# Performance work log

Hardware: AMD Instinct MI355X
Metric: run time of the kernel (lower is better)

The kernel has to match this reference:

```python
import jax, jax.numpy as jnp
import numpy as np

N_NODES = 100000
N_EDGES = 1600000
IN_DIM = 128
HID = 128
OUT_DIM = 64
EPS = 1e-8


def setup_inputs() -> dict:
    key = jax.random.key(0)
    ks = jax.random.split(key, 10)
    x = jax.random.normal(ks[0], (N_NODES, IN_DIM), dtype=jnp.float32)
    edge_index = jax.random.randint(ks[1], (2, N_EDGES), 0, N_NODES, dtype=jnp.int64)
    edge_attr = jax.random.uniform(ks[2], (N_EDGES, 4), dtype=jnp.float32)
    s1 = 1.0 / np.sqrt(IN_DIM)
    s2 = 1.0 / np.sqrt(HID)
    sr = 1.0 / np.sqrt(2 * HID)
    W1 = jax.random.normal(ks[3], (HID, IN_DIM), dtype=jnp.float32) * s1
    b1 = jnp.zeros((HID,), dtype=jnp.float32)
    W2 = jax.random.normal(ks[4], (HID, HID), dtype=jnp.float32) * s2
    b2 = jnp.zeros((HID,), dtype=jnp.float32)
    Wr = jax.random.normal(ks[5], (OUT_DIM, 2 * HID), dtype=jnp.float32) * sr
    br = jnp.zeros((OUT_DIM,), dtype=jnp.float32)
    return {"x": x, "edge_index": edge_index, "edge_attr": edge_attr,
            "W1": W1, "b1": b1, "W2": W2, "b2": b2, "Wr": Wr, "br": br}


def _edge_weight_from_attr_auto(edge_attr):
    # mean over features, min-max normalize, invert, clamp >= 0
    m = edge_attr.mean(axis=-1)                      # [E]
    m_min, m_max = m.min(), m.max()
    m_norm = (m - m_min) / (m_max - m_min + EPS)
    w = jnp.where(m_max - m_min > EPS, 1.0 - m_norm, jnp.ones_like(m))
    return jnp.clip(w, 0.0)


def reference(x, edge_index, edge_attr, W1, b1, W2, b2, Wr, br):
    N = x.shape[0]
    row, col = edge_index[0], edge_index[1]          # source -> target
    ew = _edge_weight_from_attr_auto(edge_attr)      # [E]
    # GCN normalization with self-loops (self-loop weight = 1.0)
    deg = jax.ops.segment_sum(ew, col, num_segments=N) + 1.0   # [N]
    dis = jax.lax.rsqrt(deg)                         # deg >= 1
    norm = dis[row] * ew * dis[col]                  # [E]

    def gcn(h, W, b):
        hW = h @ W.T                                 # [N, d_out]
        agg = jax.ops.segment_sum(norm[:, None] * hW[row], col, num_segments=N)
        # self-loop contribution: dis[i] * 1.0 * dis[i] * hW[i]
        return agg + (dis * dis)[:, None] * hW + b

    # dropout in eval mode -> identity
    h1 = jax.nn.relu(gcn(x, W1, b1))                 # [N, HID]
    h2 = jax.nn.relu(gcn(h1, W2, b2))                # [N, HID]
    hcat = jnp.concatenate([h1, h2], axis=-1)        # [N, 2*HID] (JK concat)
    return hcat @ Wr.T + br                          # residue-level [N, OUT_DIM]
```

## Files before the change

kernel.cpp:

```cpp
#include <hip/hip_runtime.h>

#define NN 100000
#define NE 1600000
#define HID 128
#define ODIM 64
#define NBK 196
#define BSHIFT 9
#define BINB 200
#define CVTB 8
#define GEMMB 782
#define CHUNK 8000
#define BITER 8
#define BINCAP 12288
#define SMAX 8588
#define LMAX 2148

typedef unsigned int u32;
typedef unsigned short u16;
typedef __bf16 bf16x8 __attribute__((ext_vector_type(8)));
typedef float f32x4 __attribute__((ext_vector_type(4)));
typedef float f32x2 __attribute__((ext_vector_type(2)));

__device__ __forceinline__ float bf_lo(u32 p){ return __uint_as_float(p << 16); }
__device__ __forceinline__ float bf_hi(u32 p){ return __uint_as_float(p & 0xffff0000u); }
__device__ __forceinline__ u16 f2bf(float f){
  u32 u = __float_as_uint(f);
  u += 0x7fffu + ((u >> 16) & 1u);
  return (u16)(u >> 16);
}
__device__ __forceinline__ bf16x8 ld8bf(const u16* p){ return *(const bf16x8*)p; }
__device__ __forceinline__ bf16x8 cvt8(const float* p){
  union { bf16x8 v; u16 s[8]; } r;
#pragma unroll
  for (int i = 0; i < 8; i++) r.s[i] = f2bf(p[i]);
  return r.v;
}

__device__ __forceinline__ void wparams(const u32* minmax, float* A, float* B){
  u32 mnq = 32767u - minmax[0];
  u32 mxq = minmax[1];
  u32 rngq = mxq - mnq;
  float inv = rngq ? 1.f / ((float)rngq * (1.f / 32767.f) + 1e-8f) : 0.f;
  *A = 1.f + (float)mnq * (1.f / 32767.f) * inv;
  *B = inv * (1.f / 32767.f);
}

__global__ __launch_bounds__(1024, 8) void k_front(
    const float* __restrict__ eattr, const int* __restrict__ erow,
    const int* __restrict__ ecol, u32* __restrict__ bcur,
    u32* __restrict__ binA, u16* __restrict__ binM, u32* __restrict__ minmax,
    const float* __restrict__ x, const float* __restrict__ W1,
    const float* __restrict__ W2, const float* __restrict__ Wr,
    u16* __restrict__ W2b, u16* __restrict__ Wrb, u16* __restrict__ graw){
  int tid = threadIdx.x;
  int bid = blockIdx.x;
  if (bid >= BINB + CVTB){
    int gblk = bid - BINB - CVTB;
    int wv = tid >> 6, lane = tid & 63;
    int mg = wv >> 2, ng = wv & 3;
    int m0 = gblk * 128 + mg * 32;
    int m = lane & 15, q = lane >> 4;
    const float* a0f = x + (size_t)min(m0 + m, NN - 1) * HID;
    const float* a1f = x + (size_t)min(m0 + 16 + m, NN - 1) * HID;
    const float* brow0 = W1 + (size_t)(ng * 16 + m) * HID;
    const float* brow1 = brow0 + (size_t)64 * HID;
    f32x4 acc00 = {0.f,0.f,0.f,0.f}, acc01 = {0.f,0.f,0.f,0.f};
    f32x4 acc10 = {0.f,0.f,0.f,0.f}, acc11 = {0.f,0.f,0.f,0.f};
#pragma unroll
    for (int kb = 0; kb < HID; kb += 32){
      bf16x8 af0 = cvt8(a0f + kb + q * 8);
      bf16x8 af1 = cvt8(a1f + kb + q * 8);
      bf16x8 bf0 = cvt8(brow0 + kb + q * 8);
      bf16x8 bf1 = cvt8(brow1 + kb + q * 8);
      acc00 = __builtin_amdgcn_mfma_f32_16x16x32_bf16(af0, bf0, acc00, 0, 0, 0);
      acc01 = __builtin_amdgcn_mfma_f32_16x16x32_bf16(af0, bf1, acc01, 0, 0, 0);
      acc10 = __builtin_amdgcn_mfma_f32_16x16x32_bf16(af1, bf0, acc10, 0, 0, 0);
      acc11 = __builtin_amdgcn_mfma_f32_16x16x32_bf16(af1, bf1, acc11, 0, 0, 0);
    }
#pragma unroll
    for (int r = 0; r < 4; r++){
      int row0 = m0 + q * 4 + r, row1 = m0 + 16 + q * 4 + r;
      if (row0 < NN){
        u16* c0 = graw + (size_t)row0 * HID + ng * 16 + m;
        c0[0]  = f2bf(acc00[r]);
        c0[64] = f2bf(acc01[r]);
      }
      if (row1 < NN){
        u16* c1 = graw + (size_t)row1 * HID + ng * 16 + m;
        c1[0]  = f2bf(acc10[r]);
        c1[64] = f2bf(acc11[r]);
      }
    }
    return;
  }
  if (bid >= BINB){
    int i = (bid - BINB) * 1024 + tid;
    const float* src; u16* dst; int off;
    if (i < 4096){ src = W2; dst = W2b; off = i; }
    else { src = Wr; dst = Wrb; off = i - 4096; }
    float4 v = ((const float4*)src)[off];
    uint2 o;
    o.x = (u32)f2bf(v.x) | ((u32)f2bf(v.y) << 16);
    o.y = (u32)f2bf(v.z) | ((u32)f2bf(v.w) << 16);
    ((uint2*)dst)[off] = o;
    return;
  }
  __shared__ u32 lcnt[8 * NBK], wof[8 * NBK];
  __shared__ u32 lofs[NBK], gb[NBK];
  __shared__ u32 wtot[4];
  __shared__ u16 lmap[LMAX];
  __shared__ u32 stageA[SMAX];
  __shared__ u16 stageM[SMAX];
  __shared__ u32 Tt;
  __shared__ u32 sMn[16], sMx[16];
  for (int t = tid; t < 8 * NBK; t += 1024) lcnt[t] = 0;
  __syncthreads();
  int base = bid * CHUNK;
  int wv = tid >> 6, lane = tid & 63;
  int grp = tid >> 7;
  u32 pk[BITER];
#pragma unroll
  for (int it = 0; it < BITER; it++){
    int idx = it * 1024 + tid;
    u32 p = 0xFFFFFFFFu;
    if (idx < CHUNK){
      int c = ecol[base + idx];
      if ((u32)c < NN){
        u32 b = (u32)c >> BSHIFT;
        u32 r = atomicAdd(&lcnt[grp * NBK + b], 1u);
        p = (b << 22) | (((u32)c & 511u) << 13) | r;
      }
    }
    pk[it] = p;
  }
  __syncthreads();
  u32 na = 0;
  if (tid < NBK){
    u32 run = 0;
#pragma unroll
    for (int g = 0; g < 8; g++){
      wof[g * NBK + tid] = run;
      run += lcnt[g * NBK + tid];
    }
    na = (run + 3u) & ~3u;
    lofs[tid] = run;
  }
  u32 incl = na;
  if (tid < 256){
    for (int off = 1; off < 64; off <<= 1){
      u32 t = (u32)__shfl_up((int)incl, off);
      if (lane >= off) incl += t;
    }
    if (lane == 63) wtot[wv] = incl;
  }
  __syncthreads();
  if (tid < 256){
    u32 pre = 0;
#pragma unroll
    for (int k = 0; k < 4; k++) pre += (k < wv) ? wtot[k] : 0u;
    u32 ex = pre + incl - na;
    if (tid == 255) Tt = pre + incl;
    if (tid < NBK){
      u32 n = lofs[tid];
      lofs[tid] = ex;
      u32 g = 0x80000000u;
      if (na){
        u32 gl = atomicAdd(&bcur[tid], na);
        if (gl + na <= BINCAP) g = (u32)tid * BINCAP + gl;
      }
      gb[tid] = g;
      for (u32 l = ex >> 2; l < (ex + na) >> 2; l++) lmap[l] = (u16)tid;
      for (u32 k = n; k < na; k++){ stageA[ex + k] = 0xFFFFFFFFu; stageM[ex + k] = 0; }
    }
  }
  __syncthreads();
  u32 lmn = 0, lmx = 0;
#pragma unroll
  for (int it = 0; it < BITER; it++){
    int idx = it * 1024 + tid;
    if (idx >= CHUNK) continue;
    int e = base + idx;
    float4 a = ((const float4*)eattr)[e];
    float m = 0.25f * (a.x + a.y + a.z + a.w);
    u32 mq = (u32)(m * 32767.f + 0.5f);
    lmn = max(lmn, 32767u - mq); lmx = max(lmx, mq);
    u32 p = pk[it];
    if (p == 0xFFFFFFFFu) continue;
    u32 s = (u32)erow[e]; if (s >= NN) s = 0;
    u32 b = p >> 22, d = (p >> 13) & 511u, r = p & 8191u;
    u32 slot = lofs[b] + wof[grp * NBK + b] + r;
    stageA[slot] = s | (d << 17);
    stageM[slot] = (u16)mq;
  }
  __syncthreads();
  u32 T = Tt;
  for (u32 i = tid; i < T; i += 1024){
    u32 b = lmap[i >> 2];
    u32 g = gb[b];
    if (g != 0x80000000u){
      u32 o = g + (i - lofs[b]);
      binA[o] = stageA[i];
      binM[o] = stageM[i];
    }
  }
  for (int off = 32; off; off >>= 1){
    lmn = max(lmn, (u32)__shfl_xor((int)lmn, off));
    lmx = max(lmx, (u32)__shfl_xor((int)lmx, off));
  }
  if (lane == 0){ sMn[wv] = lmn; sMx[wv] = lmx; }
  __syncthreads();
  if (tid == 0){
    u32 mn = 0, mx = 0;
#pragma unroll
    for (int k = 0; k < 16; k++){ mn = max(mn, sMn[k]); mx = max(mx, sMx[k]); }
    atomicMax(&minmax[0], mn);
    atomicMax(&minmax[1], mx);
  }
}

__global__ __launch_bounds__(1024) void k_scatter(
    const u32* __restrict__ bcur, const u32* __restrict__ binA,
    const u16* __restrict__ binM, const u32* __restrict__ minmax,
    u32* __restrict__ csr, u32* __restrict__ meta, float* __restrict__ dis){
  __shared__ u32 cntL[512], sumL[512], curL[512];
  __shared__ u32 wtot[8];
  int b = blockIdx.x, tid = threadIdx.x;
  int bb = b * BINCAP;
  int nrec = (int)min(bcur[b], (u32)BINCAP);
  if (tid < 512){ cntL[tid] = 0; sumL[tid] = 0; }
  __syncthreads();
  for (int i = tid; i < nrec; i += 1024){
    u32 a = binA[bb + i];
    if (a == 0xFFFFFFFFu) continue;
    u32 d = (a >> 17) & 511u;
    u32 mq = binM[bb + i];
    atomicAdd(&cntL[d], 1u);
    atomicAdd(&sumL[d], mq);
  }
  __syncthreads();
  float A, B; wparams(minmax, &A, &B);
  int wid = tid >> 6, lane = tid & 63;
  u32 v = 0, incl = 0;
  if (tid < 512){ v = cntL[tid]; incl = v; }
  for (int off = 1; off < 64; off <<= 1){
    u32 t = (u32)__shfl_up((int)incl, off);
    if (lane >= off) incl += t;
  }
  if (tid < 512 && lane == 63) wtot[wid] = incl;
  __syncthreads();
  if (tid < 512){
    u32 pre = 0;
#pragma unroll
    for (int k = 0; k < 8; k++) pre += (k < wid) ? wtot[k] : 0u;
    u32 ex = pre + incl - v;
    curL[tid] = (u32)bb + ex;
    int node = (b << BSHIFT) + tid;
    if (node < NN){
      meta[node] = ((u32)bb + ex) | (v << 22);
      float sw = A * (float)v - B * (float)sumL[tid];
      dis[node] = rsqrtf(1.f + sw);
    }
  }
  __syncthreads();
  for (int i = tid; i < nrec; i += 1024){
    u32 a = binA[bb + i];
    if (a == 0xFFFFFFFFu) continue;
    u32 d = (a >> 17) & 511u;
    u32 mq = binM[bb + i];
    u32 pos = atomicAdd(&curL[d], 1u);
    csr[pos] = (a & 0x1FFFFu) | (mq << 17);
  }
}

__global__ __launch_bounds__(256) void k_gemm128(
    const u16* __restrict__ Ab, const u16* __restrict__ Bt,
    const float* __restrict__ dis, u16* __restrict__ G){
  int wave = threadIdx.x >> 6, lane = threadIdx.x & 63;
  int m0 = blockIdx.x * 32;
  int m = lane & 15, q = lane >> 4;
  const u16* a0b = Ab + (size_t)(m0 + m) * HID;
  const u16* a1b = a0b + (size_t)16 * HID;
  const u16* brow0 = Bt + (size_t)(wave * 16 + m) * HID;
  const u16* brow1 = brow0 + (size_t)64 * HID;
  f32x4 acc00 = {0.f,0.f,0.f,0.f}, acc01 = {0.f,0.f,0.f,0.f};
  f32x4 acc10 = {0.f,0.f,0.f,0.f}, acc11 = {0.f,0.f,0.f,0.f};
#pragma unroll
  for (int kb = 0; kb < HID; kb += 32){
    bf16x8 af0 = ld8bf(a0b + kb + q * 8);
    bf16x8 af1 = ld8bf(a1b + kb + q * 8);
    bf16x8 bf0 = ld8bf(brow0 + kb + q * 8);
    bf16x8 bf1 = ld8bf(brow1 + kb + q * 8);
    acc00 = __builtin_amdgcn_mfma_f32_16x16x32_bf16(af0, bf0, acc00, 0, 0, 0);
    acc01 = __builtin_amdgcn_mfma_f32_16x16x32_bf16(af0, bf1, acc01, 0, 0, 0);
    acc10 = __builtin_amdgcn_mfma_f32_16x16x32_bf16(af1, bf0, acc10, 0, 0, 0);
    acc11 = __builtin_amdgcn_mfma_f32_16x16x32_bf16(af1, bf1, acc11, 0, 0, 0);
  }
  u16* crow0 = G + (size_t)(m0 + q * 4) * HID + wave * 16 + m;
  u16* crow1 = crow0 + (size_t)16 * HID;
#pragma unroll
  for (int r = 0; r < 4; r++){
    float d0 = dis[m0 + q * 4 + r];
    float d1 = dis[m0 + 16 + q * 4 + r];
    crow0[(size_t)r * HID]      = f2bf(acc00[r] * d0);
    crow0[(size_t)r * HID + 64] = f2bf(acc01[r] * d0);
    crow1[(size_t)r * HID]      = f2bf(acc10[r] * d1);
    crow1[(size_t)r * HID + 64] = f2bf(acc11[r] * d1);
  }
}

template <bool FD>
__global__ __launch_bounds__(256) void k_aggregate(
    const u32* __restrict__ meta, const u32* __restrict__ csr,
    const float* __restrict__ dis, const u32* __restrict__ minmax,
    const u16* __restrict__ g, const float* __restrict__ bias,
    u16* __restrict__ hout){
  int node = __builtin_amdgcn_readfirstlane(
      (int)(blockIdx.x * 4 + (threadIdx.x >> 6)));
  int lane = threadIdx.x & 63;
  const u32* gp = (const u32*)g;
  u32 sv = gp[((size_t)node << 6) + lane];
  u32 mw = meta[node];
  float di = dis[node];
  float A, B; wparams(minmax, &A, &B);
  u32 s = mw & 0x3FFFFFu;
  int c = (int)(mw >> 22);
  const u32* cp = csr + s;
  f32x2 acc = {0.f, 0.f};
  int j = 0;
  for (; j + 16 <= c; j += 16){
    u32 p[16];
#pragma unroll
    for (int t = 0; t < 16; t++)
      p[t] = __builtin_amdgcn_readfirstlane(cp[j + t]);
    u32 pv[16];
#pragma unroll
    for (int t = 0; t < 16; t++)
      pv[t] = gp[(size_t)(p[t] & 0x1FFFFu) * 64u + lane];
#pragma unroll
    for (int t = 0; t < 16; t++){
      float wf = A - B * (float)(p[t] >> 17);
      if (FD) wf *= dis[p[t] & 0x1FFFFu];
      f32x2 val = {bf_lo(pv[t]), bf_hi(pv[t])};
      f32x2 w2 = {wf, wf};
      acc += w2 * val;
    }
  }
  for (; j < c; j += 8){
    u32 p[8];
#pragma unroll
    for (int t = 0; t < 8; t++)
      p[t] = __builtin_amdgcn_readfirstlane(cp[j + t]);
    u32 st[8]; float wv[8];
#pragma unroll
    for (int t = 0; t < 8; t++){
      bool ok = (j + t) < c;
      st[t] = ok ? (p[t] & 0x1FFFFu) : 0u;
      float wf = A - B * (float)(p[t] >> 17);
      if (FD) wf *= dis[st[t]];
      wv[t] = ok ? wf : 0.f;
    }
    u32 pv[8];
#pragma unroll
    for (int t = 0; t < 8; t++)
      pv[t] = gp[(size_t)st[t] * 64u + lane];
#pragma unroll
    for (int t = 0; t < 8; t++){
      f32x2 val = {bf_lo(pv[t]), bf_hi(pv[t])};
      f32x2 w2 = {wv[t], wv[t]};
      acc += w2 * val;
    }
  }
  float2 bv = ((const float2*)bias)[lane];
  f32x2 selfv = {bf_lo(sv), bf_hi(sv)};
  float sc = FD ? di : 1.f;
  float o0 = fmaxf((acc.x + sc * selfv.x) * di + bv.x, 0.f);
  float o1 = fmaxf((acc.y + sc * selfv.y) * di + bv.y, 0.f);
  ((u32*)hout)[((size_t)node << 6) + lane] = (u32)f2bf(o0) | ((u32)f2bf(o1) << 16);
}

__global__ __launch_bounds__(256) void k_readout(
    const u16* __restrict__ h1, const u16* __restrict__ h2,
    const u16* __restrict__ Wrb, const float* __restrict__ br, float* __restrict__ out){
  int wave = threadIdx.x >> 6, lane = threadIdx.x & 63;
  int m0 = blockIdx.x * 32;
  int n0 = wave * 16;
  int m = lane & 15, q = lane >> 4;
  const u16* a10 = h1 + (size_t)(m0 + m) * HID;
  const u16* a11 = a10 + (size_t)16 * HID;
  const u16* a20 = h2 + (size_t)(m0 + m) * HID;
  const u16* a21 = a20 + (size_t)16 * HID;
  const u16* b  = Wrb + (size_t)(n0 + m) * (2 * HID);
  f32x4 acc0 = {0.f,0.f,0.f,0.f}, acc1 = {0.f,0.f,0.f,0.f};
#pragma unroll
  for (int kb = 0; kb < HID; kb += 32){
    bf16x8 bf = ld8bf(b + kb + q * 8);
    acc0 = __builtin_amdgcn_mfma_f32_16x16x32_bf16(ld8bf(a10 + kb + q * 8), bf, acc0, 0, 0, 0);
    acc1 = __builtin_amdgcn_mfma_f32_16x16x32_bf16(ld8bf(a11 + kb + q * 8), bf, acc1, 0, 0, 0);
  }
#pragma unroll
  for (int kb = 0; kb < HID; kb += 32){
    bf16x8 bf = ld8bf(b + HID + kb + q * 8);
    acc0 = __builtin_amdgcn_mfma_f32_16x16x32_bf16(ld8bf(a20 + kb + q * 8), bf, acc0, 0, 0, 0);
    acc1 = __builtin_amdgcn_mfma_f32_16x16x32_bf16(ld8bf(a21 + kb + q * 8), bf, acc1, 0, 0, 0);
  }
  float bias = br[n0 + m];
  float* crow0 = out + (size_t)(m0 + q * 4) * ODIM + n0 + m;
  float* crow1 = crow0 + (size_t)16 * ODIM;
#pragma unroll
  for (int r = 0; r < 4; r++){
    crow0[(size_t)r * ODIM] = acc0[r] + bias;
    crow1[(size_t)r * ODIM] = acc1[r] + bias;
  }
}

extern "C" void kernel_launch(void* const* d_in, const int* in_sizes, int n_in,
                              void* d_out, int out_size, void* d_ws, size_t ws_size,
                              hipStream_t stream){
  const float* x     = (const float*)d_in[0];
  const int*   eidx  = (const int*)d_in[1];
  const float* eattr = (const float*)d_in[2];
  const float* W1    = (const float*)d_in[3];
  const float* b1    = (const float*)d_in[4];
  const float* W2    = (const float*)d_in[5];
  const float* b2    = (const float*)d_in[6];
  const float* Wr    = (const float*)d_in[7];
  const float* br    = (const float*)d_in[8];
  const int* erow  = eidx;
  const int* ecol  = eidx + NE;

  char* w = (char*)d_ws;
  auto carve = [&](size_t bytes) -> void* {
    void* p = (void*)w;
    w += (bytes + 255) & ~(size_t)255;
    return p;
  };
  u32* csr       = (u32*)carve((size_t)NBK * BINCAP * 4);
  u32* bcur      = (u32*)carve(1024);
  u32* minmax    = (u32*)carve(256);
  u32* meta      = (u32*)carve((size_t)NN * 4);
  float* dis     = (float*)carve((size_t)NN * 4);
  u16* W2b       = (u16*)carve((size_t)HID * HID * 2);
  u16* Wrb       = (u16*)carve((size_t)ODIM * 2 * HID * 2);
  u16* g         = (u16*)carve((size_t)NN * HID * 2);
  u16* h1        = (u16*)carve((size_t)NN * HID * 2);
  u16* h2        = (u16*)carve((size_t)NN * HID * 2);
  u32* binA      = (u32*)h2;
  u16* binM      = (u16*)((char*)h2 + (size_t)NBK * BINCAP * 4);

  hipMemsetAsync(bcur, 0, 1280, stream);
  k_front<<<BINB + CVTB + GEMMB, 1024, 0, stream>>>(
      eattr, erow, ecol, bcur, binA, binM, minmax,
      x, W1, W2, Wr, W2b, Wrb, g);
  k_scatter<<<NBK, 1024, 0, stream>>>(bcur, binA, binM, minmax, csr, meta, dis);
  k_aggregate<true><<<NN / 4, 256, 0, stream>>>(meta, csr, dis, minmax, g, b1, h1);
  k_gemm128<<<NN / 32, 256, 0, stream>>>(h1, W2b, dis, g);
  k_aggregate<false><<<NN / 4, 256, 0, stream>>>(meta, csr, dis, minmax, g, b2, h2);
  k_readout<<<NN / 32, 256, 0, stream>>>(h1, h2, Wrb, br, (float*)d_out);
}
```

Baseline: 374.3 us.

## Fuse second aggregation with readout GEMM and pack bin records into uint2

Replaces the second aggregate kernel and the readout GEMM with one kernel. Each 1024-thread block aggregates 16 nodes, stages the h1 and h2 rows in shared memory, and runs the MFMA readout there, so h2 is never written to or re-read from global memory. Bin records are now stored as interleaved uint2 (index plus weight) instead of two separate arrays, and scatter histograms are split into four per-group copies to reduce LDS atomic contention. The cost is a larger bin buffer, a block-wide barrier before the readout, and only 4 of 16 waves doing the MFMA work.

Result: faster. 356.3 us (-4.8%).

```diff
diff --git a/kernel.cpp b/kernel.cpp
--- a/kernel.cpp
+++ b/kernel.cpp
@@ -48,7 +48,7 @@
 __global__ __launch_bounds__(1024, 8) void k_front(
     const float* __restrict__ eattr, const int* __restrict__ erow,
     const int* __restrict__ ecol, u32* __restrict__ bcur,
-    u32* __restrict__ binA, u16* __restrict__ binM, u32* __restrict__ minmax,
+    uint2* __restrict__ bin8, u32* __restrict__ minmax,
     const float* __restrict__ x, const float* __restrict__ W1,
     const float* __restrict__ W2, const float* __restrict__ Wr,
     u16* __restrict__ W2b, u16* __restrict__ Wrb, u16* __restrict__ graw){
@@ -198,9 +198,8 @@
     u32 b = lmap[i >> 2];
     u32 g = gb[b];
     if (g != 0x80000000u){
-      u32 o = g + (i - lofs[b]);
-      binA[o] = stageA[i];
-      binM[o] = stageM[i];
+      uint2 rec; rec.x = stageA[i]; rec.y = (u32)stageM[i];
+      bin8[g + (i - lofs[b])] = rec;
     }
   }
   for (int off = 32; off; off >>= 1){
@@ -219,29 +218,34 @@
 }
 
 __global__ __launch_bounds__(1024) void k_scatter(
-    const u32* __restrict__ bcur, const u32* __restrict__ binA,
-    const u16* __restrict__ binM, const u32* __restrict__ minmax,
-    u32* __restrict__ csr, u32* __restrict__ meta, float* __restrict__ dis){
-  __shared__ u32 cntL[512], sumL[512], curL[512];
+    const u32* __restrict__ bcur, const uint2* __restrict__ bin8,
+    const u32* __restrict__ minmax, u32* __restrict__ csr,
+    u32* __restrict__ meta, float* __restrict__ dis){
+  __shared__ u32 cnt4[4 * 512], sum4[4 * 512];
+  __shared__ u32 curL[512];
   __shared__ u32 wtot[8];
   int b = blockIdx.x, tid = threadIdx.x;
+  int grp = tid >> 8;
   int bb = b * BINCAP;
   int nrec = (int)min(bcur[b], (u32)BINCAP);
-  if (tid < 512){ cntL[tid] = 0; sumL[tid] = 0; }
+  for (int t = tid; t < 4 * 512; t += 1024){ cnt4[t] = 0; sum4[t] = 0; }
   __syncthreads();
   for (int i = tid; i < nrec; i += 1024){
-    u32 a = binA[bb + i];
-    if (a == 0xFFFFFFFFu) continue;
-    u32 d = (a >> 17) & 511u;
-    u32 mq = binM[bb + i];
-    atomicAdd(&cntL[d], 1u);
-    atomicAdd(&sumL[d], mq);
+    uint2 r = bin8[bb + i];
+    if (r.x == 0xFFFFFFFFu) continue;
+    u32 d = (r.x >> 17) & 511u;
+    atomicAdd(&cnt4[grp * 512 + d], 1u);
+    atomicAdd(&sum4[grp * 512 + d], r.y);
   }
   __syncthreads();
   float A, B; wparams(minmax, &A, &B);
   int wid = tid >> 6, lane = tid & 63;
-  u32 v = 0, incl = 0;
-  if (tid < 512){ v = cntL[tid]; incl = v; }
+  u32 v = 0, sm = 0, incl = 0;
+  if (tid < 512){
+    v  = cnt4[tid] + cnt4[512 + tid] + cnt4[1024 + tid] + cnt4[1536 + tid];
+    sm = sum4[tid] + sum4[512 + tid] + sum4[1024 + tid] + sum4[1536 + tid];
+    incl = v;
+  }
   for (int off = 1; off < 64; off <<= 1){
     u32 t = (u32)__shfl_up((int)incl, off);
     if (lane >= off) incl += t;
@@ -257,18 +261,17 @@
     int node = (b << BSHIFT) + tid;
     if (node < NN){
       meta[node] = ((u32)bb + ex) | (v << 22);
-      float sw = A * (float)v - B * (float)sumL[tid];
+      float sw = A * (float)v - B * (float)sm;
       dis[node] = rsqrtf(1.f + sw);
     }
   }
   __syncthreads();
   for (int i = tid; i < nrec; i += 1024){
-    u32 a = binA[bb + i];
-    if (a == 0xFFFFFFFFu) continue;
-    u32 d = (a >> 17) & 511u;
-    u32 mq = binM[bb + i];
+    uint2 r = bin8[bb + i];
+    if (r.x == 0xFFFFFFFFu) continue;
+    u32 d = (r.x >> 17) & 511u;
     u32 pos = atomicAdd(&curL[d], 1u);
-    csr[pos] = (a & 0x1FFFFu) | (mq << 17);
+    csr[pos] = (r.x & 0x1FFFFu) | (r.y << 17);
   }
 }
 
@@ -308,7 +311,6 @@
   }
 }
 
-template <bool FD>
 __global__ __launch_bounds__(256) void k_aggregate(
     const u32* __restrict__ meta, const u32* __restrict__ csr,
     const float* __restrict__ dis, const u32* __restrict__ minmax,
@@ -338,8 +340,7 @@
       pv[t] = gp[(size_t)(p[t] & 0x1FFFFu) * 64u + lane];
 #pragma unroll
     for (int t = 0; t < 16; t++){
-      float wf = A - B * (float)(p[t] >> 17);
-      if (FD) wf *= dis[p[t] & 0x1FFFFu];
+      float wf = (A - B * (float)(p[t] >> 17)) * dis[p[t] & 0x1FFFFu];
       f32x2 val = {bf_lo(pv[t]), bf_hi(pv[t])};
       f32x2 w2 = {wf, wf};
       acc += w2 * val;
@@ -355,9 +356,7 @@
     for (int t = 0; t < 8; t++){
       bool ok = (j + t) < c;
       st[t] = ok ? (p[t] & 0x1FFFFu) : 0u;
-      float wf = A - B * (float)(p[t] >> 17);
-      if (FD) wf *= dis[st[t]];
-      wv[t] = ok ? wf : 0.f;
+      wv[t] = ok ? (A - B * (float)(p[t] >> 17)) * dis[st[t]] : 0.f;
     }
     u32 pv[8];
 #pragma unroll
@@ -372,44 +371,93 @@
   }
   float2 bv = ((const float2*)bias)[lane];
   f32x2 selfv = {bf_lo(sv), bf_hi(sv)};
-  float sc = FD ? di : 1.f;
-  float o0 = fmaxf((acc.x + sc * selfv.x) * di + bv.x, 0.f);
-  float o1 = fmaxf((acc.y + sc * selfv.y) * di + bv.y, 0.f);
+  float o0 = fmaxf((acc.x + di * selfv.x) * di + bv.x, 0.f);
+  float o1 = fmaxf((acc.y + di * selfv.y) * di + bv.y, 0.f);
   ((u32*)hout)[((size_t)node << 6) + lane] = (u32)f2bf(o0) | ((u32)f2bf(o1) << 16);
 }
 
-__global__ __launch_bounds__(256) void k_readout(
-    const u16* __restrict__ h1, const u16* __restrict__ h2,
-    const u16* __restrict__ Wrb, const float* __restrict__ br, float* __restrict__ out){
-  int wave = threadIdx.x >> 6, lane = threadIdx.x & 63;
-  int m0 = blockIdx.x * 32;
-  int n0 = wave * 16;
-  int m = lane & 15, q = lane >> 4;
-  const u16* a10 = h1 + (size_t)(m0 + m) * HID;
-  const u16* a11 = a10 + (size_t)16 * HID;
-  const u16* a20 = h2 + (size_t)(m0 + m) * HID;
-  const u16* a21 = a20 + (size_t)16 * HID;
-  const u16* b  = Wrb + (size_t)(n0 + m) * (2 * HID);
-  f32x4 acc0 = {0.f,0.f,0.f,0.f}, acc1 = {0.f,0.f,0.f,0.f};
-#pragma unroll
-  for (int kb = 0; kb < HID; kb += 32){
-    bf16x8 bf = ld8bf(b + kb + q * 8);
-    acc0 = __builtin_amdgcn_mfma_f32_16x16x32_bf16(ld8bf(a10 + kb + q * 8), bf, acc0, 0, 0, 0);
-    acc1 = __builtin_amdgcn_mfma_f32_16x16x32_bf16(ld8bf(a11 + kb + q * 8), bf, acc1, 0, 0, 0);
-  }
-#pragma unroll
-  for (int kb = 0; kb < HID; kb += 32){
-    bf16x8 bf = ld8bf(b + HID + kb + q * 8);
-    acc0 = __builtin_amdgcn_mfma_f32_16x16x32_bf16(ld8bf(a20 + kb + q * 8), bf, acc0, 0, 0, 0);
-    acc1 = __builtin_amdgcn_mfma_f32_16x16x32_bf16(ld8bf(a21 + kb + q * 8), bf, acc1, 0, 0, 0);
-  }
-  float bias = br[n0 + m];
-  float* crow0 = out + (size_t)(m0 + q * 4) * ODIM + n0 + m;
-  float* crow1 = crow0 + (size_t)16 * ODIM;
-#pragma unroll
-  for (int r = 0; r < 4; r++){
-    crow0[(size_t)r * ODIM] = acc0[r] + bias;
-    crow1[(size_t)r * ODIM] = acc1[r] + bias;
+__global__ __launch_bounds__(1024) void k_agg_read(
+    const u32* __restrict__ meta, const u32* __restrict__ csr,
+    const float* __restrict__ dis, const u32* __restrict__ minmax,
+    const u16* __restrict__ g, const float* __restrict__ bias,
+    const u16* __restrict__ h1, const u16* __restrict__ Wrb,
+    const float* __restrict__ br, float* __restrict__ out){
+  __shared__ u16 hc[16][264];
+  int wv = threadIdx.x >> 6, lane = threadIdx.x & 63;
+  int node0 = blockIdx.x * 16;
+  int node = __builtin_amdgcn_readfirstlane(node0 + wv);
+  const u32* gp = (const u32*)g;
+  u32 sv = gp[((size_t)node << 6) + lane];
+  u32 mw = meta[node];
+  float di = dis[node];
+  float A, B; wparams(minmax, &A, &B);
+  u32 s = mw & 0x3FFFFFu;
+  int c = (int)(mw >> 22);
+  const u32* cp = csr + s;
+  f32x2 acc = {0.f, 0.f};
+  int j = 0;
+  for (; j + 16 <= c; j += 16){
+    u32 p[16];
+#pragma unroll
+    for (int t = 0; t < 16; t++)
+      p[t] = __builtin_amdgcn_readfirstlane(cp[j + t]);
+    u32 pv[16];
+#pragma unroll
+    for (int t = 0; t < 16; t++)
+      pv[t] = gp[(size_t)(p[t] & 0x1FFFFu) * 64u + lane];
+#pragma unroll
+    for (int t = 0; t < 16; t++){
+      float wf = A - B * (float)(p[t] >> 17);
+      f32x2 val = {bf_lo(pv[t]), bf_hi(pv[t])};
+      f32x2 w2 = {wf, wf};
+      acc += w2 * val;
+    }
+  }
+  for (; j < c; j += 8){
+    u32 p[8];
+#pragma unroll
+    for (int t = 0; t < 8; t++)
+      p[t] = __builtin_amdgcn_readfirstlane(cp[j + t]);
+    u32 st[8]; float wvv[8];
+#pragma unroll
+    for (int t = 0; t < 8; t++){
+      bool ok = (j + t) < c;
+      st[t] = ok ? (p[t] & 0x1FFFFu) : 0u;
+      wvv[t] = ok ? (A - B * (float)(p[t] >> 17)) : 0.f;
+    }
+    u32 pv[8];
+#pragma unroll
+    for (int t = 0; t < 8; t++)
+      pv[t] = gp[(size_t)st[t] * 64u + lane];
+#pragma unroll
+    for (int t = 0; t < 8; t++){
+      f32x2 val = {bf_lo(pv[t]), bf_hi(pv[t])};
+      f32x2 w2 = {wvv[t], wvv[t]};
+      acc += w2 * val;
+    }
+  }
+  float2 bv = ((const float2*)bias)[lane];
+  f32x2 selfv = {bf_lo(sv), bf_hi(sv)};
+  float o0 = fmaxf((acc.x + selfv.x) * di + bv.x, 0.f);
+  float o1 = fmaxf((acc.y + selfv.y) * di + bv.y, 0.f);
+  u32 h2pk = (u32)f2bf(o0) | ((u32)f2bf(o1) << 16);
+  *(u32*)&hc[wv][2 * lane] = ((const u32*)h1)[((size_t)node << 6) + lane];
+  *(u32*)&hc[wv][128 + 2 * lane] = h2pk;
+  __syncthreads();
+  if (wv < 4){
+    int m = lane & 15, q = lane >> 4;
+    const u16* b = Wrb + (size_t)(wv * 16 + m) * (2 * HID);
+    f32x4 acc4 = {0.f,0.f,0.f,0.f};
+#pragma unroll
+    for (int kb = 0; kb < 2 * HID; kb += 32){
+      bf16x8 af = *(const bf16x8*)&hc[m][kb + q * 8];
+      bf16x8 bf = ld8bf(b + kb + q * 8);
+      acc4 = __builtin_amdgcn_mfma_f32_16x16x32_bf16(af, bf, acc4, 0, 0, 0);
+    }
+    float bb = br[wv * 16 + m];
+#pragma unroll
+    for (int r = 0; r < 4; r++)
+      out[(size_t)(node0 + q * 4 + r) * ODIM + wv * 16 + m] = acc4[r] + bb;
   }
 }
 
@@ -443,17 +491,15 @@
   u16* Wrb       = (u16*)carve((size_t)ODIM * 2 * HID * 2);
   u16* g         = (u16*)carve((size_t)NN * HID * 2);
   u16* h1        = (u16*)carve((size_t)NN * HID * 2);
-  u16* h2        = (u16*)carve((size_t)NN * HID * 2);
-  u32* binA      = (u32*)h2;
-  u16* binM      = (u16*)((char*)h2 + (size_t)NBK * BINCAP * 4);
+  uint2* bin8    = (uint2*)carve((size_t)NBK * BINCAP * 8);
 
   hipMemsetAsync(bcur, 0, 1280, stream);
   k_front<<<BINB + CVTB + GEMMB, 1024, 0, stream>>>(
-      eattr, erow, ecol, bcur, binA, binM, minmax,
+      eattr, erow, ecol, bcur, bin8, minmax,
       x, W1, W2, Wr, W2b, Wrb, g);
-  k_scatter<<<NBK, 1024, 0, stream>>>(bcur, binA, binM, minmax, csr, meta, dis);
-  k_aggregate<true><<<NN / 4, 256, 0, stream>>>(meta, csr, dis, minmax, g, b1, h1);
+  k_scatter<<<NBK, 1024, 0, stream>>>(bcur, bin8, minmax, csr, meta, dis);
+  k_aggregate<<<NN / 4, 256, 0, stream>>>(meta, csr, dis, minmax, g, b1, h1);
   k_gemm128<<<NN / 32, 256, 0, stream>>>(h1, W2b, dis, g);
-  k_aggregate<false><<<NN / 4, 256, 0, stream>>>(meta, csr, dis, minmax, g, b2, h2);
-  k_readout<<<NN / 32, 256, 0, stream>>>(h1, h2, Wrb, br, (float*)d_out);
-}
+  k_agg_read<<<NN / 16, 1024, 0, stream>>>(meta, csr, dis, minmax, g, b2,
+                                           h1, Wrb, br, (float*)d_out);
+}
```
